# Kernel tuning notes

Hardware: AMD Instinct MI355X
Metric: run time of the kernel (lower is better)

The kernel has to match this reference:

```python
import jax, jax.numpy as jnp
import numpy as np


def log_g(x):
    # log of g(x) = x + 0.5 for x>=0, sigmoid(x) for x<0
    return jnp.where(x >= 0, jnp.log(jax.nn.relu(x) + 0.5), -jax.nn.softplus(-x))


def setup_inputs() -> dict:
    key = jax.random.key(0)
    k1, k2 = jax.random.split(key)
    B, S, D = 4, 4096, 1024
    x = jax.random.normal(k1, (B, S, D), dtype=jnp.float32)
    # nn.Linear(dim, 2*dim, bias=False) weight: [2*dim, dim], scaled like kaiming-uniform-ish
    W = jax.random.normal(k2, (2 * D, D), dtype=jnp.float32) * (1.0 / np.sqrt(D))
    return {"x": x, "W": W}


def reference(x, W):
    # x: [B, S, D], W: [2D, D] -> hidden, gate: [B, S, D]
    hg = jnp.einsum("bsd,ed->bse", x, W)
    hidden, gate = jnp.split(hg, 2, axis=-1)

    log_coeffs = -jax.nn.softplus(gate)        # log(1 - z)
    log_z = -jax.nn.softplus(-gate)            # log(z)
    log_values = log_z + log_g(hidden)

    # Heinsen associative scan in log space along seq axis
    a_star = jnp.cumsum(log_coeffs, axis=1)
    log_h0_plus_b_star = jax.lax.cumlogsumexp(log_values - a_star, axis=1)
    log_h = a_star + log_h0_plus_b_star
    out = jnp.exp(log_h)                       # [B, S, D]
    # expansion_factor == 1.0 -> to_out is Identity
    return out
```

## Files before the change

### kernel.cpp

```cpp
#include <hip/hip_runtime.h>
#include <hip/hip_bf16.h>
#include <hip/hip_fp16.h>
#include <math.h>

#define B_  4
#define S_  4096
#define D_  1024
#define M_  (B_ * S_)
#define K_  D_
#define L_  32
#define NC_ (S_ / L_)
#define NKT 32

typedef __attribute__((ext_vector_type(8))) short          bf16x8;
typedef __attribute__((ext_vector_type(8))) unsigned short u16x8;
typedef __attribute__((ext_vector_type(4))) float          f32x4;

__device__ __forceinline__ unsigned short f2bf(float f) {
    union { __hip_bfloat16 h; unsigned short u; } cv;
    cv.h = __float2bfloat16(f);
    return cv.u;
}

__device__ __forceinline__ float fast_rcp(float x) {
#if __has_builtin(__builtin_amdgcn_rcpf)
    return __builtin_amdgcn_rcpf(x);
#else
    return 1.0f / x;
#endif
}

__device__ __forceinline__ void stage16(const unsigned short* src, char* dst) {
    __builtin_amdgcn_global_load_lds(
        (const __attribute__((address_space(1))) unsigned int*)src,
        (__attribute__((address_space(3))) unsigned int*)dst, 16, 0, 0);
}

__global__ __launch_bounds__(256) void to_bf16(
    const float* __restrict__ in, unsigned short* __restrict__ out, int n8)
{
    int i = blockIdx.x * 256 + threadIdx.x;
    if (i >= n8) return;
    const float4* p = (const float4*)in + (size_t)i * 2;
    float4 a = p[0], b = p[1];
    u16x8 o;
    o[0] = f2bf(a.x); o[1] = f2bf(a.y); o[2] = f2bf(a.z); o[3] = f2bf(a.w);
    o[4] = f2bf(b.x); o[5] = f2bf(b.y); o[6] = f2bf(b.z); o[7] = f2bf(b.w);
    *(u16x8*)(out + (size_t)i * 8) = o;
}

__global__ __launch_bounds__(256, 1) void gemm_pointwise(
    const unsigned short* __restrict__ xb, const unsigned short* __restrict__ Wb,
    __half2* __restrict__ cvb, float2* __restrict__ CVagg)
{
    __shared__ char lds[131072];

    const int th   = threadIdx.x;
    const int lane = th & 63;
    const int wave = th >> 6;
    const int wm = wave >> 1;
    const int wn = wave & 1;

    const int wg  = blockIdx.x;
    const int swz = (wg & 7) * 64 + (wg >> 3);
    const int m0 = (swz >> 3) * 256;
    const int d0 = (swz & 7) * 128;

    f32x4 acc[8][8];
#pragma unroll
    for (int i = 0; i < 8; ++i)
#pragma unroll
        for (int j = 0; j < 8; ++j)
            acc[i][j] = (f32x4){0.f, 0.f, 0.f, 0.f};

    const int srow = th >> 2;
    const int scol = (((th & 3) ^ ((th >> 3) & 3)) * 8);
    const unsigned short* srcA  = xb + (size_t)(m0 + srow)      * K_ + scol;
    const unsigned short* srcBh = Wb + (size_t)(d0 + srow)      * K_ + scol;
    const unsigned short* srcBg = Wb + (size_t)(D_ + d0 + srow) * K_ + scol;
    char* const wuo = lds + wave * 1024;

    const int lr = lane & 15;
    const int lq = lane >> 4;
    const int lkb = ((lq ^ ((lr >> 1) & 3)) * 16);
    const int aoffb = (wm * 128 + lr) * 64 + lkb;
    const int boffb = 16384 + (wn * 64 + lr) * 64 + lkb;

    bf16x8 Af[8], Bf[8];

#define BAR()  asm volatile("s_barrier" ::: "memory")
#define VMW(n) asm volatile("s_waitcnt vmcnt(" #n ")" ::: "memory")

#define STAGE(tt) do { const int ko_ = (tt) * 32;                        \
    char* d_ = wuo + ((tt) & 3) * 32768;                                 \
    stage16(srcA  + ko_,              d_);                               \
    stage16(srcA  + 64 * K_  + ko_,   d_ + 4096);                        \
    stage16(srcA  + 128 * K_ + ko_,   d_ + 8192);                        \
    stage16(srcA  + 192 * K_ + ko_,   d_ + 12288);                       \
    stage16(srcBh + ko_,              d_ + 16384);                       \
    stage16(srcBh + 64 * K_  + ko_,   d_ + 20480);                       \
    stage16(srcBg + ko_,              d_ + 24576);                       \
    stage16(srcBg + 64 * K_  + ko_,   d_ + 28672);                       \
  } while (0)

#define TILEBODY(T, PRE, WAITOP) do {                                     \
    const char* bc_ = lds + ((T) & 3) * 32768;                            \
    _Pragma("unroll")                                                     \
    for (int i_ = 0; i_ < 8; ++i_)                                        \
        Af[i_] = *(const bf16x8*)(bc_ + aoffb + i_ * 1024);               \
    _Pragma("unroll")                                                     \
    for (int j_ = 0; j_ < 4; ++j_) {                                      \
        Bf[j_]     = *(const bf16x8*)(bc_ + boffb + j_ * 1024);           \
        Bf[j_ + 4] = *(const bf16x8*)(bc_ + boffb + 8192 + j_ * 1024);    \
    }                                                                     \
    if (PRE) { STAGE((T) + 3); }                                          \
    _Pragma("unroll")                                                     \
    for (int i_ = 0; i_ < 8; ++i_)                                        \
        _Pragma("unroll")                                                 \
        for (int j_ = 0; j_ < 8; ++j_)                                    \
            acc[i_][j_] = __builtin_amdgcn_mfma_f32_16x16x32_bf16(        \
                Af[i_], Bf[j_], acc[i_][j_], 0, 0, 0);                    \
    WAITOP;                                                               \
    BAR();                                                                \
  } while (0)

    STAGE(0); STAGE(1); STAGE(2);
    VMW(16);
    BAR();

#pragma unroll 1
    for (int t = 0; t < NKT - 3; ++t)
        TILEBODY(t, 1, VMW(16));
    TILEBODY(NKT - 3, 0, VMW(8));
    TILEBODY(NKT - 2, 0, VMW(0));
    TILEBODY(NKT - 1, 0, (void)0);

#undef TILEBODY
#undef STAGE
#undef BAR
#undef VMW

#pragma unroll
    for (int mp = 0; mp < 4; ++mp) {
        float C16[2][4], V16[2][4];
#pragma unroll
        for (int hf = 0; hf < 2; ++hf) {
            const int mi = mp * 2 + hf;
#pragma unroll
            for (int nj = 0; nj < 4; ++nj) {
                float C4 = 1.0f, V4 = 0.0f;
                const int d = d0 + wn * 64 + nj * 16 + lr;
#pragma unroll
                for (int r = 0; r < 4; ++r) {
                    int m = m0 + wm * 128 + mi * 16 + lq * 4 + r;
                    float h = acc[mi][nj][r];
                    float g = acc[mi][nj + 4][r];
                    float eg  = __expf(g);
                    float c   = fast_rcp(1.0f + eg);
                    float z   = eg * c;
                    float enh = __expf(-h);
                    float sh  = fast_rcp(1.0f + enh);
                    float gh  = (h >= 0.0f) ? (h + 0.5f) : sh;
                    float v   = z * gh;
                    cvb[(size_t)m * D_ + d] = __floats2half2_rn(c, v);
                    V4 = fmaf(c, V4, v);
                    C4 *= c;
                }
                float Ca = __shfl_xor(C4, 16), Va = __shfl_xor(V4, 16);
                float Clo = (lq & 1) ? Ca : C4, Vlo = (lq & 1) ? Va : V4;
                float Chi = (lq & 1) ? C4 : Ca, Vhi = (lq & 1) ? V4 : Va;
                float C2 = Clo * Chi, V2 = fmaf(Chi, Vlo, Vhi);
                float Cb = __shfl_xor(C2, 32), Vb = __shfl_xor(V2, 32);
                float Cl2 = (lq & 2) ? Cb : C2, Vl2 = (lq & 2) ? Vb : V2;
                float Ch2 = (lq & 2) ? C2 : Cb, Vh2 = (lq & 2) ? V2 : Vb;
                C16[hf][nj] = Cl2 * Ch2;
                V16[hf][nj] = fmaf(Ch2, Vl2, Vh2);
            }
        }
        if (lq == 0) {
            const int chunkg = (m0 + wm * 128 + mp * 32) >> 5;
#pragma unroll
            for (int nj = 0; nj < 4; ++nj) {
                float C32 = C16[0][nj] * C16[1][nj];
                float V32 = fmaf(C16[1][nj], V16[0][nj], V16[1][nj]);
                const int d = d0 + wn * 64 + nj * 16 + lr;
                float2 st; st.x = C32; st.y = V32;
                CVagg[(size_t)chunkg * D_ + d] = st;
            }
        }
    }
}

__global__ __launch_bounds__(256) void chunk_scan(
    const float2* __restrict__ CVagg, float* __restrict__ P)
{
    const int d = blockIdx.x * 256 + threadIdx.x;
    const int b = blockIdx.z;
    float h = 0.0f;
    for (int c = 0; c < NC_; ++c) {
        size_t o = ((size_t)b * NC_ + c) * D_ + d;
        P[o] = h;
        float2 cv = CVagg[o];
        h = fmaf(cv.x, h, cv.y);
    }
}

__global__ __launch_bounds__(256) void chunk_apply(
    const unsigned int* __restrict__ cvw, const float* __restrict__ P,
    float* __restrict__ out)
{
    const int d = (blockIdx.x * 256 + threadIdx.x) * 2;
    const int c = blockIdx.y;
    const int b = blockIdx.z;
    size_t base = ((size_t)(b * S_ + c * L_)) * D_ + d;
    float2 h2 = *(const float2*)(P + ((size_t)b * NC_ + c) * D_ + d);
    float h0 = h2.x, h1 = h2.y;
    for (int s = 0; s < L_; ++s) {
        uint2 u = *(const uint2*)(cvw + base + (size_t)s * D_);
        float2 p0 = __half22float2(*(const __half2*)&u.x);
        float2 p1 = __half22float2(*(const __half2*)&u.y);
        h0 = fmaf(p0.x, h0, p0.y);
        h1 = fmaf(p1.x, h1, p1.y);
        float2 o2 = {h0, h1};
        *(float2*)(out + base + (size_t)s * D_) = o2;
    }
}

extern "C" void kernel_launch(void* const* d_in, const int* in_sizes, int n_in,
                              void* d_out, int out_size, void* d_ws, size_t ws_size,
                              hipStream_t stream) {
    const float* x = (const float*)d_in[0];
    const float* W = (const float*)d_in[1];
    float* out = (float*)d_out;

    float2* CVagg = (float2*)d_ws;
    float*  P     = (float*)(CVagg + (size_t)B_ * NC_ * D_);
    __half2* cvb  = (__half2*)(P + (size_t)B_ * NC_ * D_);
    unsigned short* xb = (unsigned short*)(cvb + (size_t)M_ * D_);
    unsigned short* Wb = xb + (size_t)M_ * K_;

    const int nx8 = M_ * K_ / 8;
    const int nw8 = 2 * D_ * K_ / 8;
    to_bf16<<<(nx8 + 255) / 256, 256, 0, stream>>>(x, xb, nx8);
    to_bf16<<<(nw8 + 255) / 256, 256, 0, stream>>>(W, Wb, nw8);

    gemm_pointwise<<<512, 256, 0, stream>>>(xb, Wb, cvb, CVagg);

    dim3 g3(D_ / 256, 1, B_);
    chunk_scan<<<g3, 256, 0, stream>>>(CVagg, P);

    dim3 g2(D_ / 512, NC_, B_);
    chunk_apply<<<g2, 256, 0, stream>>>((const unsigned int*)cvb, P, out);
}
```

Baseline: 135.8 us.

## Halve GEMM M-tile for two blocks per CU, split MFMA phases, merge bf16 casts

Shrinks the GEMM workgroup tile from 256 to 128 rows, cutting accumulators and LDS (triple buffering in 72KB) so two workgroups can share a CU, and doubles the grid to 1024 blocks. The k-loop is split into a hidden phase and a gate phase, each with its own loads, barriers and raised wave priority around the MFMAs, to interleave LDS reads with compute. The two fp32-to-bf16 conversion launches are merged into one kernel to save a launch. The trade-off is less operand reuse per tile, more barriers per k-step, and a shallower prefetch depth.

```diff
diff --git a/kernel.cpp b/kernel.cpp
--- a/kernel.cpp
+++ b/kernel.cpp
@@ -36,24 +36,34 @@
         (__attribute__((address_space(3))) unsigned int*)dst, 16, 0, 0);
 }
 
-__global__ __launch_bounds__(256) void to_bf16(
-    const float* __restrict__ in, unsigned short* __restrict__ out, int n8)
+__global__ __launch_bounds__(256) void to_bf16_both(
+    const float* __restrict__ x, const float* __restrict__ W,
+    unsigned short* __restrict__ xb, unsigned short* __restrict__ Wb,
+    int n8x, int n8w)
 {
     int i = blockIdx.x * 256 + threadIdx.x;
-    if (i >= n8) return;
-    const float4* p = (const float4*)in + (size_t)i * 2;
+    const float* src;
+    unsigned short* dst;
+    int j;
+    if (i < n8x) { src = x; dst = xb; j = i; }
+    else {
+        j = i - n8x;
+        if (j >= n8w) return;
+        src = W; dst = Wb;
+    }
+    const float4* p = (const float4*)src + (size_t)j * 2;
     float4 a = p[0], b = p[1];
     u16x8 o;
     o[0] = f2bf(a.x); o[1] = f2bf(a.y); o[2] = f2bf(a.z); o[3] = f2bf(a.w);
     o[4] = f2bf(b.x); o[5] = f2bf(b.y); o[6] = f2bf(b.z); o[7] = f2bf(b.w);
-    *(u16x8*)(out + (size_t)i * 8) = o;
-}
-
-__global__ __launch_bounds__(256, 1) void gemm_pointwise(
+    *(u16x8*)(dst + (size_t)j * 8) = o;
+}
+
+__global__ __launch_bounds__(256, 2) void gemm_pointwise(
     const unsigned short* __restrict__ xb, const unsigned short* __restrict__ Wb,
     __half2* __restrict__ cvb, float2* __restrict__ CVagg)
 {
-    __shared__ char lds[131072];
+    __shared__ char lds[73728];
 
     const int th   = threadIdx.x;
     const int lane = th & 63;
@@ -62,13 +72,13 @@
     const int wn = wave & 1;
 
     const int wg  = blockIdx.x;
-    const int swz = (wg & 7) * 64 + (wg >> 3);
-    const int m0 = (swz >> 3) * 256;
+    const int swz = (wg & 7) * 128 + (wg >> 3);
+    const int m0 = (swz >> 3) * 128;
     const int d0 = (swz & 7) * 128;
 
-    f32x4 acc[8][8];
-#pragma unroll
-    for (int i = 0; i < 8; ++i)
+    f32x4 acc[4][8];
+#pragma unroll
+    for (int i = 0; i < 4; ++i)
 #pragma unroll
         for (int j = 0; j < 8; ++j)
             acc[i][j] = (f32x4){0.f, 0.f, 0.f, 0.f};
@@ -83,65 +93,93 @@
     const int lr = lane & 15;
     const int lq = lane >> 4;
     const int lkb = ((lq ^ ((lr >> 1) & 3)) * 16);
-    const int aoffb = (wm * 128 + lr) * 64 + lkb;
-    const int boffb = 16384 + (wn * 64 + lr) * 64 + lkb;
-
-    bf16x8 Af[8], Bf[8];
+    const int aoffb = (wm * 64 + lr) * 64 + lkb;
+    const int boffh = 8192 + (wn * 64 + lr) * 64 + lkb;
+    const int boffg = boffh + 8192;
+
+    bf16x8 Af[4], Bf[8];
 
 #define BAR()  asm volatile("s_barrier" ::: "memory")
-#define VMW(n) asm volatile("s_waitcnt vmcnt(" #n ")" ::: "memory")
-
-#define STAGE(tt) do { const int ko_ = (tt) * 32;                        \
-    char* d_ = wuo + ((tt) & 3) * 32768;                                 \
-    stage16(srcA  + ko_,              d_);                               \
-    stage16(srcA  + 64 * K_  + ko_,   d_ + 4096);                        \
-    stage16(srcA  + 128 * K_ + ko_,   d_ + 8192);                        \
-    stage16(srcA  + 192 * K_ + ko_,   d_ + 12288);                       \
-    stage16(srcBh + ko_,              d_ + 16384);                       \
-    stage16(srcBh + 64 * K_  + ko_,   d_ + 20480);                       \
-    stage16(srcBg + ko_,              d_ + 24576);                       \
-    stage16(srcBg + 64 * K_  + ko_,   d_ + 28672);                       \
-  } while (0)
-
-#define TILEBODY(T, PRE, WAITOP) do {                                     \
-    const char* bc_ = lds + ((T) & 3) * 32768;                            \
-    _Pragma("unroll")                                                     \
-    for (int i_ = 0; i_ < 8; ++i_)                                        \
-        Af[i_] = *(const bf16x8*)(bc_ + aoffb + i_ * 1024);               \
-    _Pragma("unroll")                                                     \
-    for (int j_ = 0; j_ < 4; ++j_) {                                      \
-        Bf[j_]     = *(const bf16x8*)(bc_ + boffb + j_ * 1024);           \
-        Bf[j_ + 4] = *(const bf16x8*)(bc_ + boffb + 8192 + j_ * 1024);    \
-    }                                                                     \
-    if (PRE) { STAGE((T) + 3); }                                          \
-    _Pragma("unroll")                                                     \
-    for (int i_ = 0; i_ < 8; ++i_)                                        \
+#define LGK0() asm volatile("s_waitcnt lgkmcnt(0)" ::: "memory")
+#define VMW6() asm volatile("s_waitcnt vmcnt(6)" ::: "memory")
+#define VMW0() asm volatile("s_waitcnt vmcnt(0)" ::: "memory")
+
+#define STAGE_AH(tt, q) do { const int ko_ = (tt) * 32;                   \
+    stage16(srcA  + ko_,            (q));                                 \
+    stage16(srcA  + 64 * K_ + ko_,  (q) + 4096);                          \
+    stage16(srcBh + ko_,            (q) + 8192);                          \
+    stage16(srcBh + 64 * K_ + ko_,  (q) + 12288); } while (0)
+#define STAGE_G(tt, q) do { const int ko_ = (tt) * 32;                    \
+    stage16(srcBg + ko_,            (q) + 16384);                         \
+    stage16(srcBg + 64 * K_ + ko_,  (q) + 20480); } while (0)
+
+#define TILEBODY(T, P0, Q2, PRE, WAITOP) do {                             \
+    _Pragma("unroll")                                                     \
+    for (int i_ = 0; i_ < 4; ++i_)                                        \
+        Af[i_] = *(const bf16x8*)((P0) + aoffb + i_ * 1024);              \
+    _Pragma("unroll")                                                     \
+    for (int j_ = 0; j_ < 4; ++j_)                                        \
+        Bf[j_] = *(const bf16x8*)((P0) + boffh + j_ * 1024);              \
+    if (PRE) { STAGE_AH((T) + 2, (Q2)); }                                 \
+    BAR(); LGK0();                                                        \
+    __builtin_amdgcn_s_setprio(1);                                        \
+    _Pragma("unroll")                                                     \
+    for (int i_ = 0; i_ < 4; ++i_)                                        \
         _Pragma("unroll")                                                 \
-        for (int j_ = 0; j_ < 8; ++j_)                                    \
+        for (int j_ = 0; j_ < 4; ++j_)                                    \
             acc[i_][j_] = __builtin_amdgcn_mfma_f32_16x16x32_bf16(        \
                 Af[i_], Bf[j_], acc[i_][j_], 0, 0, 0);                    \
+    __builtin_amdgcn_s_setprio(0);                                        \
+    BAR();                                                                \
+    _Pragma("unroll")                                                     \
+    for (int j_ = 0; j_ < 4; ++j_)                                        \
+        Bf[4 + j_] = *(const bf16x8*)((P0) + boffg + j_ * 1024);          \
+    if (PRE) { STAGE_G((T) + 2, (Q2)); }                                  \
+    BAR(); LGK0();                                                        \
+    __builtin_amdgcn_s_setprio(1);                                        \
+    _Pragma("unroll")                                                     \
+    for (int i_ = 0; i_ < 4; ++i_)                                        \
+        _Pragma("unroll")                                                 \
+        for (int j_ = 0; j_ < 4; ++j_)                                    \
+            acc[i_][4 + j_] = __builtin_amdgcn_mfma_f32_16x16x32_bf16(    \
+                Af[i_], Bf[4 + j_], acc[i_][4 + j_], 0, 0, 0);            \
+    __builtin_amdgcn_s_setprio(0);                                        \
     WAITOP;                                                               \
     BAR();                                                                \
   } while (0)
 
-    STAGE(0); STAGE(1); STAGE(2);
-    VMW(16);
+    const char* p0 = lds;
+    const char* p1 = lds + 24576;
+    const char* p2 = lds + 49152;
+    char* q0 = wuo;
+    char* q1 = wuo + 24576;
+    char* q2 = wuo + 49152;
+
+    STAGE_AH(0, q0); STAGE_G(0, q0);
+    STAGE_AH(1, q1); STAGE_G(1, q1);
+    VMW6();
     BAR();
 
 #pragma unroll 1
-    for (int t = 0; t < NKT - 3; ++t)
-        TILEBODY(t, 1, VMW(16));
-    TILEBODY(NKT - 3, 0, VMW(8));
-    TILEBODY(NKT - 2, 0, VMW(0));
-    TILEBODY(NKT - 1, 0, (void)0);
+    for (int t = 0; t < NKT - 2; ++t) {
+        TILEBODY(t, p0, q2, 1, VMW6());
+        const char* tp = p0; p0 = p1; p1 = p2; p2 = tp;
+        char* tq = q0; q0 = q1; q1 = q2; q2 = tq;
+    }
+    TILEBODY(NKT - 2, p0, q2, 0, VMW0());
+    { const char* tp = p0; p0 = p1; p1 = p2; p2 = tp; }
+    TILEBODY(NKT - 1, p0, q2, 0, (void)0);
 
 #undef TILEBODY
-#undef STAGE
+#undef STAGE_AH
+#undef STAGE_G
 #undef BAR
-#undef VMW
-
-#pragma unroll
-    for (int mp = 0; mp < 4; ++mp) {
+#undef LGK0
+#undef VMW6
+#undef VMW0
+
+#pragma unroll
+    for (int mp = 0; mp < 2; ++mp) {
         float C16[2][4], V16[2][4];
 #pragma unroll
         for (int hf = 0; hf < 2; ++hf) {
@@ -152,7 +190,7 @@
                 const int d = d0 + wn * 64 + nj * 16 + lr;
 #pragma unroll
                 for (int r = 0; r < 4; ++r) {
-                    int m = m0 + wm * 128 + mi * 16 + lq * 4 + r;
+                    int m = m0 + wm * 64 + mi * 16 + lq * 4 + r;
                     float h = acc[mi][nj][r];
                     float g = acc[mi][nj + 4][r];
                     float eg  = __expf(g);
@@ -178,7 +216,7 @@
             }
         }
         if (lq == 0) {
-            const int chunkg = (m0 + wm * 128 + mp * 32) >> 5;
+            const int chunkg = (m0 + wm * 64 + mp * 32) >> 5;
 #pragma unroll
             for (int nj = 0; nj < 4; ++nj) {
                 float C32 = C16[0][nj] * C16[1][nj];
@@ -239,12 +277,11 @@
     unsigned short* xb = (unsigned short*)(cvb + (size_t)M_ * D_);
     unsigned short* Wb = xb + (size_t)M_ * K_;
 
-    const int nx8 = M_ * K_ / 8;
-    const int nw8 = 2 * D_ * K_ / 8;
-    to_bf16<<<(nx8 + 255) / 256, 256, 0, stream>>>(x, xb, nx8);
-    to_bf16<<<(nw8 + 255) / 256, 256, 0, stream>>>(W, Wb, nw8);
-
-    gemm_pointwise<<<512, 256, 0, stream>>>(xb, Wb, cvb, CVagg);
+    const int n8x = M_ * K_ / 8;
+    const int n8w = 2 * D_ * K_ / 8;
+    to_bf16_both<<<(n8x + n8w + 255) / 256, 256, 0, stream>>>(x, W, xb, Wb, n8x, n8w);
+
+    gemm_pointwise<<<1024, 256, 0, stream>>>(xb, Wb, cvb, CVagg);
 
     dim3 g3(D_ / 256, 1, B_);
     chunk_scan<<<g3, 256, 0, stream>>>(CVagg, P);
```

New measurement: 129.8 us. -4.4%, faster.
